# Optimization experiments

Hardware: AMD Instinct MI355X
Metric: run time of the kernel (lower is better)

The kernel has to match this reference:

```python
import jax, jax.numpy as jnp
import numpy as np

N = 2_000_000   # total flattened logits (anchors x classes scale)
FG = 256        # number of foreground (targets==1) entries
DELTA = 1.0


def setup_inputs() -> dict:
    key = jax.random.key(0)
    k1, k2 = jax.random.split(key)
    logits = jax.random.normal(k1, (N,), dtype=jnp.float32)
    fg_idx = jax.random.choice(k2, N, shape=(FG,), replace=False)
    targets = jnp.zeros((N,), dtype=jnp.int32).at[fg_idx].set(1)
    return {"logits": logits, "targets": targets, "fg_num": FG}


def _ap_loss(logits, targets, fg_num):
    """Faithful port of AP_loss: returns (loss [1], grad [N]).

    The torch validity filter (targets==0 & logits >= min(fg)-delta) is
    redundant: for invalid bg, (l - fg_i)/(2*delta)+0.5 < 0, so clamp gives 0.
    We therefore mask with (targets==0) over the full array (static shapes).
    """
    bg_mask = (targets == 0).astype(logits.dtype)
    fg_idx = jnp.nonzero(targets == 1, size=fg_num)[0]
    fg_logits = logits[fg_idx]            # [fg]
    order = jnp.argsort(fg_logits)
    sorted_fg = fg_logits[order]          # ascending, matches torch loop order

    inv2d = 1.0 / (2.0 * DELTA)

    def step(carry, f_i):
        max_prec, bg_grad = carry
        tmp1 = jnp.clip((fg_logits - f_i) * inv2d + 0.5, 0.0, 1.0)   # [fg]
        tmp2 = jnp.clip((logits - f_i) * inv2d + 0.5, 0.0, 1.0) * bg_mask  # [N]
        a = jnp.sum(tmp1) + 0.5
        b = jnp.sum(tmp2)
        cur = a / (a + b)
        new_max = jnp.maximum(max_prec, cur)
        scale = jnp.where(max_prec <= cur, 1.0, (1.0 - max_prec) / (1.0 - cur))
        bg_grad = bg_grad + tmp2 * (scale / (a + b))
        return (new_max, bg_grad), new_max

    init = (jnp.zeros((), logits.dtype), jnp.zeros_like(logits))
    (_, bg_grad), prec_sorted = jax.lax.scan(step, init, sorted_fg)

    prec = jnp.zeros((fg_num,), logits.dtype).at[order].set(prec_sorted)
    grad = bg_grad.at[fg_idx].set(-(1.0 - prec))
    denom = max(fg_num, 1)
    grad = grad / denom
    metric = jnp.sum(prec, keepdims=True) / denom   # [1]
    return 1.0 - metric, grad


def reference(logits, targets, fg_num):
    loss, _ = _ap_loss(logits, targets, fg_num)
    return loss
```

## Files before the change

### kernel.cpp

```cpp
#include <hip/hip_runtime.h>

#define FG    256
#define NBIN  1024
#define BINV  32.0f
#define BOFF  512.0f
#define NBLK  256

typedef unsigned long long u64;
typedef unsigned int u32;


__global__ void __launch_bounds__(1024) hist_kernel(
        const float* __restrict__ logits,
        const int* __restrict__ targets,
        float* __restrict__ fgslots,
        int* __restrict__ fgcnt,
        u32* __restrict__ partials, int n) {
    __shared__ u32 h[NBIN];
    __shared__ float lfg[FG];
    __shared__ int lcnt;
    const int tid = threadIdx.x;
    h[tid] = 0u;
    if (tid == 0) lcnt = 0;
    __syncthreads();

    const int n4 = n >> 2;
    const float4* l4 = (const float4*)logits;
    const int4*   t4 = (const int4*)targets;
    const int stride = gridDim.x * blockDim.x;
    for (int i = blockIdx.x * blockDim.x + tid; i < n4; i += stride) {
        float4 x = l4[i];
        int4   t = t4[i];
        #pragma unroll
        for (int e = 0; e < 4; ++e) {
            float l  = (e == 0) ? x.x : (e == 1) ? x.y : (e == 2) ? x.z : x.w;
            int   tg = (e == 0) ? t.x : (e == 1) ? t.y : (e == 2) ? t.z : t.w;
            float u = fmaf(l, BINV, BOFF);
            u = fminf(fmaxf(u, 0.f), 1023.99f);
            int b = (int)u;
            u32 qoff = (u32)((u - (float)b) * 32.0f);
            atomicAdd(&h[b], (1u << 18) | qoff);
            if (tg == 1) {
                int p = atomicAdd(&lcnt, 1);
                if (p < FG) lfg[p] = l;
            }
        }
    }
    if (blockIdx.x == 0 && tid == 0) {
        for (int i = n4 << 2; i < n; ++i) {
            float l = logits[i];
            float u = fmaf(l, BINV, BOFF);
            u = fminf(fmaxf(u, 0.f), 1023.99f);
            int b = (int)u;
            u32 qoff = (u32)((u - (float)b) * 32.0f);
            atomicAdd(&h[b], (1u << 18) | qoff);
            if (targets[i] == 1) {
                int p = atomicAdd(&lcnt, 1);
                if (p < FG) lfg[p] = l;
            }
        }
    }
    __syncthreads();
    partials[blockIdx.x * NBIN + tid] = h[tid];
    const int c = (lcnt < FG) ? lcnt : FG;
    if (tid == 0) fgcnt[blockIdx.x] = c;
    if (tid < c) fgslots[blockIdx.x * FG + tid] = lfg[tid];
}

__global__ void __launch_bounds__(1024) final_kernel(
        const int* __restrict__ fgcnt,
        const float* __restrict__ fgslots,
        const u32* __restrict__ partials,
        float* __restrict__ out, int n) {
    __shared__ float rc[NBIN], rs[NBIN];
    __shared__ float pc[NBIN], ps[NBIN];
    __shared__ float sfv[FG], sf[FG];
    __shared__ int   pr[1024];
    __shared__ float pa[1024];
    __shared__ float wc[16], ws[16];
    __shared__ float wm[4], wsum[4];
    __shared__ u32   ucnt[NBIN], uqs[NBIN];
    __shared__ int   fwp[4];
    const int tid  = threadIdx.x;
    const int lane = tid & 63;
    const int wv   = tid >> 6;

    ucnt[tid] = 0u; uqs[tid] = 0u;
    int fv = (tid < FG) ? fgcnt[tid] : 0;
    __syncthreads();

    {
        const uint4* p4 = (const uint4*)partials;
        u32 c0=0,c1=0,c2=0,c3=0,q0=0,q1=0,q2=0,q3=0;
        #pragma unroll 8
        for (int k = 0; k < 64; ++k) {
            uint4 v = p4[tid + (k << 10)];
            c0 += v.x >> 18; q0 += v.x & 0x3FFFFu;
            c1 += v.y >> 18; q1 += v.y & 0x3FFFFu;
            c2 += v.z >> 18; q2 += v.z & 0x3FFFFu;
            c3 += v.w >> 18; q3 += v.w & 0x3FFFFu;
        }
        const int bb = (tid & 255) << 2;
        atomicAdd(&ucnt[bb + 0], c0); atomicAdd(&uqs[bb + 0], q0);
        atomicAdd(&ucnt[bb + 1], c1); atomicAdd(&uqs[bb + 1], q1);
        atomicAdd(&ucnt[bb + 2], c2); atomicAdd(&uqs[bb + 2], q2);
        atomicAdd(&ucnt[bb + 3], c3); atomicAdd(&uqs[bb + 3], q3);
    }
    int fs = fv;
    if (tid < FG) {
        #pragma unroll
        for (int off = 1; off < 64; off <<= 1) {
            int t = __shfl_up(fs, off, 64);
            if (lane >= off) fs += t;
        }
        if (lane == 63) fwp[wv] = fs;
    }
    __syncthreads();

    {
        float cnt = (float)ucnt[tid];
        float qs  = (float)uqs[tid];
        float binlo = ((float)tid - BOFF) * (1.0f / BINV);
        rc[tid] = cnt;
        rs[tid] = fmaf(qs + 0.5f * cnt, 1.0f / 1024.0f, binlo * cnt);
    }
    if (tid < FG) {
        int excl = fs - fv;
        for (int w = 0; w < wv; ++w) excl += fwp[w];
        for (int j = 0; j < fv; ++j) sfv[excl + j] = fgslots[tid * FG + j];
    }
    __syncthreads();

    float c = rc[tid], s = rs[tid];
    #pragma unroll
    for (int off = 1; off < 64; off <<= 1) {
        float tc = __shfl_up(c, off, 64), ts = __shfl_up(s, off, 64);
        if (lane >= off) { c += tc; s += ts; }
    }
    if (lane == 63) { wc[wv] = c; ws[wv] = s; }

    {
        int i = tid & 255, ch = tid >> 8;
        float v = sfv[i];
        int r = 0;
        #pragma unroll 8
        for (int j = ch * 64; j < ch * 64 + 64; ++j) {
            float o = sfv[j];
            r += (o < v || (o == v && j < i)) ? 1 : 0;
        }
        pr[tid] = r;
    }
    __syncthreads();

    if (wv == 0 && lane < 16) {
        float cc = wc[lane], ss = ws[lane];
        #pragma unroll
        for (int off = 1; off < 16; off <<= 1) {
            float tc = __shfl_up(cc, off, 64), ts = __shfl_up(ss, off, 64);
            if (lane >= off) { cc += tc; ss += ts; }
        }
        wc[lane] = cc; ws[lane] = ss;
    }
    if (tid < FG) {
        int r = pr[tid] + pr[tid + 256] + pr[tid + 512] + pr[tid + 768];
        sf[r] = sfv[tid];
    }
    __syncthreads();
    if (wv > 0) { c += wc[wv - 1]; s += ws[wv - 1]; }
    pc[tid] = c; ps[tid] = s;

    {
        int i = tid & 255, ch = tid >> 8;
        float fi = sf[i];
        float sum = 0.f;
        #pragma unroll 8
        for (int j = ch * 64; j < ch * 64 + 64; ++j) {
            float v = (sf[j] - fi) * 0.5f + 0.5f;
            sum += fminf(fmaxf(v, 0.f), 1.f);
        }
        pa[tid] = sum;
    }
    __syncthreads();

    float cur = 0.f;
    if (tid < FG) {
        const float fi = sf[tid];
        const float a = 0.5f + pa[tid] + pa[tid + 256] + pa[tid + 512] + pa[tid + 768];
        float C[2], S[2];
        #pragma unroll
        for (int q = 0; q < 2; ++q) {
            float t = (q == 0) ? (fi - 1.0f) : (fi + 1.0f);
            float u = fmaf(t, BINV, BOFF);
            u = fminf(fmaxf(u, 0.f), 1023.99f);
            float kf = floorf(u);
            int   k  = (int)kf;
            float frac = u - kf;
            C[q] = pc[k] + rc[k] * (frac - 1.0f);
            S[q] = ps[k] + rs[k] * (frac - 1.0f);
        }
        const float Cab   = (float)n - C[1];
        const float Cw    = C[1] - C[0];
        const float Sw    = S[1] - S[0];
        const float b_all = Cab + 0.5f * Sw + (0.5f - 0.5f * fi) * Cw;
        const float b_bg  = b_all - (a - 0.5f);
        cur = a / (a + b_bg);
        float m = cur;
        #pragma unroll
        for (int off = 1; off < 64; off <<= 1) {
            float t = __shfl_up(m, off, 64);
            if (lane >= off) m = fmaxf(m, t);
        }
        if (lane == 63) wm[wv] = m;
        pr[tid] = __float_as_int(m);
    }
    __syncthreads();
    if (tid < FG) {
        float m = __int_as_float(pr[tid]);
        float pmax = -1.f;
        for (int w = 0; w < 4; ++w) if (w < wv) pmax = fmaxf(pmax, wm[w]);
        m = fmaxf(m, pmax);
        float v = m;
        #pragma unroll
        for (int off = 32; off; off >>= 1) v += __shfl_down(v, off, 64);
        if (lane == 0) wsum[wv] = v;
    }
    __syncthreads();
    if (tid == 0) {
        float t = (wsum[0] + wsum[1]) + (wsum[2] + wsum[3]);
        out[0] = 1.f - t / (float)FG;
    }
}

extern "C" void kernel_launch(void* const* d_in, const int* in_sizes, int n_in,
                              void* d_out, int out_size, void* d_ws, size_t ws_size,
                              hipStream_t stream) {
    const float* logits  = (const float*)d_in[0];
    const int*   targets = (const int*)d_in[1];
    const int n = in_sizes[0];

    char*  wb       = (char*)d_ws;
    int*   fgcnt    = (int*)wb;
    float* fgslots  = (float*)(wb + 4096);
    u32*   partials = (u32*)(wb + (1 << 20));
    float* out      = (float*)d_out;

    hist_kernel<<<NBLK, 1024, 0, stream>>>(logits, targets, fgslots, fgcnt, partials, n);
    final_kernel<<<1, 1024, 0, stream>>>(fgcnt, fgslots, partials, out, n);
}
```

Baseline: 85.91 us.

## Fuse histogram and final reduction into one cooperative kernel with grid syncs

```diff
diff --git a/kernel.cpp b/kernel.cpp
--- a/kernel.cpp
+++ b/kernel.cpp
@@ -1,4 +1,7 @@
 #include <hip/hip_runtime.h>
+#include <hip/hip_cooperative_groups.h>
+
+namespace cg = cooperative_groups;
 
 #define FG    256
 #define NBIN  1024
@@ -10,16 +13,32 @@
 typedef unsigned int u32;
 
 
-__global__ void __launch_bounds__(1024) hist_kernel(
+__global__ void __launch_bounds__(1024) ap_fused(
         const float* __restrict__ logits,
         const int* __restrict__ targets,
         float* __restrict__ fgslots,
         int* __restrict__ fgcnt,
-        u32* __restrict__ partials, int n) {
+        u32* __restrict__ partials,
+        u64* __restrict__ gacc,
+        float* __restrict__ out, int n) {
     __shared__ u32 h[NBIN];
     __shared__ float lfg[FG];
     __shared__ int lcnt;
-    const int tid = threadIdx.x;
+    __shared__ u32 redc[4][4], redq[4][4];
+    __shared__ float rc[NBIN], rs[NBIN];
+    __shared__ float pc[NBIN], ps[NBIN];
+    __shared__ float sfv[FG], sf[FG];
+    __shared__ int   pr[1024];
+    __shared__ float pa[1024];
+    __shared__ float wcs[16], wss[16];
+    __shared__ float wm[4], wsum[4];
+    __shared__ int   fwp[4];
+
+    const int tid  = threadIdx.x;
+    const int lane = tid & 63;
+    const int wv   = tid >> 6;
+    const int g    = blockIdx.x;
+
     h[tid] = 0u;
     if (tid == 0) lcnt = 0;
     __syncthreads();
@@ -28,7 +47,7 @@
     const float4* l4 = (const float4*)logits;
     const int4*   t4 = (const int4*)targets;
     const int stride = gridDim.x * blockDim.x;
-    for (int i = blockIdx.x * blockDim.x + tid; i < n4; i += stride) {
+    for (int i = g * blockDim.x + tid; i < n4; i += stride) {
         float4 x = l4[i];
         int4   t = t4[i];
         #pragma unroll
@@ -46,7 +65,7 @@
             }
         }
     }
-    if (blockIdx.x == 0 && tid == 0) {
+    if (g == 0 && tid == 0) {
         for (int i = n4 << 2; i < n; ++i) {
             float l = logits[i];
             float u = fmaf(l, BINV, BOFF);
@@ -61,51 +80,54 @@
         }
     }
     __syncthreads();
-    partials[blockIdx.x * NBIN + tid] = h[tid];
-    const int c = (lcnt < FG) ? lcnt : FG;
-    if (tid == 0) fgcnt[blockIdx.x] = c;
-    if (tid < c) fgslots[blockIdx.x * FG + tid] = lfg[tid];
-}
-
-__global__ void __launch_bounds__(1024) final_kernel(
-        const int* __restrict__ fgcnt,
-        const float* __restrict__ fgslots,
-        const u32* __restrict__ partials,
-        float* __restrict__ out, int n) {
-    __shared__ float rc[NBIN], rs[NBIN];
-    __shared__ float pc[NBIN], ps[NBIN];
-    __shared__ float sfv[FG], sf[FG];
-    __shared__ int   pr[1024];
-    __shared__ float pa[1024];
-    __shared__ float wc[16], ws[16];
-    __shared__ float wm[4], wsum[4];
-    __shared__ u32   ucnt[NBIN], uqs[NBIN];
-    __shared__ int   fwp[4];
-    const int tid  = threadIdx.x;
-    const int lane = tid & 63;
-    const int wv   = tid >> 6;
-
-    ucnt[tid] = 0u; uqs[tid] = 0u;
+    partials[g * NBIN + tid] = h[tid];
+    const int c_ = (lcnt < FG) ? lcnt : FG;
+    if (tid == 0) fgcnt[g] = c_;
+    if (tid < c_) fgslots[g * FG + tid] = lfg[tid];
+
+    cg::this_grid().sync();
+
+    if (tid < 256) {
+        const uint4* p4 = (const uint4*)partials;
+        uint4 v = p4[tid * (NBIN / 4) + g];
+        u32 c0 = v.x >> 18, q0 = v.x & 0x3FFFFu;
+        u32 c1 = v.y >> 18, q1 = v.y & 0x3FFFFu;
+        u32 c2 = v.z >> 18, q2 = v.z & 0x3FFFFu;
+        u32 c3 = v.w >> 18, q3 = v.w & 0x3FFFFu;
+        #pragma unroll
+        for (int off = 32; off; off >>= 1) {
+            c0 += __shfl_down(c0, off, 64); q0 += __shfl_down(q0, off, 64);
+            c1 += __shfl_down(c1, off, 64); q1 += __shfl_down(q1, off, 64);
+            c2 += __shfl_down(c2, off, 64); q2 += __shfl_down(q2, off, 64);
+            c3 += __shfl_down(c3, off, 64); q3 += __shfl_down(q3, off, 64);
+        }
+        if (lane == 0) {
+            redc[wv][0] = c0; redq[wv][0] = q0;
+            redc[wv][1] = c1; redq[wv][1] = q1;
+            redc[wv][2] = c2; redq[wv][2] = q2;
+            redc[wv][3] = c3; redq[wv][3] = q3;
+        }
+    }
+    __syncthreads();
+    if (tid < 4) {
+        u32 cnt = redc[0][tid] + redc[1][tid] + redc[2][tid] + redc[3][tid];
+        u32 qs  = redq[0][tid] + redq[1][tid] + redq[2][tid] + redq[3][tid];
+        gacc[4 * g + tid] = ((u64)cnt << 32) | (u64)qs;
+    }
+
+    cg::this_grid().sync();
+
+    if (g != 0) return;
+
+    {
+        u64 v = gacc[tid];
+        float cnt = (float)(u32)(v >> 32);
+        float qs  = (float)(u32)(v & 0xFFFFFFFFull);
+        float binlo = ((float)tid - BOFF) * (1.0f / BINV);
+        rc[tid] = cnt;
+        rs[tid] = fmaf(qs + 0.5f * cnt, 1.0f / 1024.0f, binlo * cnt);
+    }
     int fv = (tid < FG) ? fgcnt[tid] : 0;
-    __syncthreads();
-
-    {
-        const uint4* p4 = (const uint4*)partials;
-        u32 c0=0,c1=0,c2=0,c3=0,q0=0,q1=0,q2=0,q3=0;
-        #pragma unroll 8
-        for (int k = 0; k < 64; ++k) {
-            uint4 v = p4[tid + (k << 10)];
-            c0 += v.x >> 18; q0 += v.x & 0x3FFFFu;
-            c1 += v.y >> 18; q1 += v.y & 0x3FFFFu;
-            c2 += v.z >> 18; q2 += v.z & 0x3FFFFu;
-            c3 += v.w >> 18; q3 += v.w & 0x3FFFFu;
-        }
-        const int bb = (tid & 255) << 2;
-        atomicAdd(&ucnt[bb + 0], c0); atomicAdd(&uqs[bb + 0], q0);
-        atomicAdd(&ucnt[bb + 1], c1); atomicAdd(&uqs[bb + 1], q1);
-        atomicAdd(&ucnt[bb + 2], c2); atomicAdd(&uqs[bb + 2], q2);
-        atomicAdd(&ucnt[bb + 3], c3); atomicAdd(&uqs[bb + 3], q3);
-    }
     int fs = fv;
     if (tid < FG) {
         #pragma unroll
@@ -116,14 +138,6 @@
         if (lane == 63) fwp[wv] = fs;
     }
     __syncthreads();
-
-    {
-        float cnt = (float)ucnt[tid];
-        float qs  = (float)uqs[tid];
-        float binlo = ((float)tid - BOFF) * (1.0f / BINV);
-        rc[tid] = cnt;
-        rs[tid] = fmaf(qs + 0.5f * cnt, 1.0f / 1024.0f, binlo * cnt);
-    }
     if (tid < FG) {
         int excl = fs - fv;
         for (int w = 0; w < wv; ++w) excl += fwp[w];
@@ -137,7 +151,7 @@
         float tc = __shfl_up(c, off, 64), ts = __shfl_up(s, off, 64);
         if (lane >= off) { c += tc; s += ts; }
     }
-    if (lane == 63) { wc[wv] = c; ws[wv] = s; }
+    if (lane == 63) { wcs[wv] = c; wss[wv] = s; }
 
     {
         int i = tid & 255, ch = tid >> 8;
@@ -153,20 +167,20 @@
     __syncthreads();
 
     if (wv == 0 && lane < 16) {
-        float cc = wc[lane], ss = ws[lane];
+        float cc = wcs[lane], ss = wss[lane];
         #pragma unroll
         for (int off = 1; off < 16; off <<= 1) {
             float tc = __shfl_up(cc, off, 64), ts = __shfl_up(ss, off, 64);
             if (lane >= off) { cc += tc; ss += ts; }
         }
-        wc[lane] = cc; ws[lane] = ss;
+        wcs[lane] = cc; wss[lane] = ss;
     }
     if (tid < FG) {
         int r = pr[tid] + pr[tid + 256] + pr[tid + 512] + pr[tid + 768];
         sf[r] = sfv[tid];
     }
     __syncthreads();
-    if (wv > 0) { c += wc[wv - 1]; s += ws[wv - 1]; }
+    if (wv > 0) { c += wcs[wv - 1]; s += wss[wv - 1]; }
     pc[tid] = c; ps[tid] = s;
 
     {
@@ -236,14 +250,17 @@
                               hipStream_t stream) {
     const float* logits  = (const float*)d_in[0];
     const int*   targets = (const int*)d_in[1];
-    const int n = in_sizes[0];
+    int n = in_sizes[0];
 
     char*  wb       = (char*)d_ws;
     int*   fgcnt    = (int*)wb;
     float* fgslots  = (float*)(wb + 4096);
     u32*   partials = (u32*)(wb + (1 << 20));
+    u64*   gacc     = (u64*)(wb + (1 << 21));
     float* out      = (float*)d_out;
 
-    hist_kernel<<<NBLK, 1024, 0, stream>>>(logits, targets, fgslots, fgcnt, partials, n);
-    final_kernel<<<1, 1024, 0, stream>>>(fgcnt, fgslots, partials, out, n);
+    void* args[] = { &logits, &targets, &fgslots, &fgcnt,
+                     &partials, &gacc, &out, &n };
+    hipLaunchCooperativeKernel((void*)ap_fused, dim3(NBLK), dim3(1024),
+                               args, 0, stream);
 }
```

Result: slower. 140.2 us (+63.2%).

## Split histogram partial reduction into a separate 16-block kernel

Applied to the files above, without the earlier changes.

```diff
diff --git a/kernel.cpp b/kernel.cpp
--- a/kernel.cpp
+++ b/kernel.cpp
@@ -67,45 +67,62 @@
     if (tid < c) fgslots[blockIdx.x * FG + tid] = lfg[tid];
 }
 
+__global__ void __launch_bounds__(1024) reduce_kernel(
+        const u32* __restrict__ partials,
+        u64* __restrict__ gacc) {
+    __shared__ u32 sc[16 * 64], sq[16 * 64];
+    const int tid = threadIdx.x;
+    const int b  = tid & 63;
+    const int r0 = tid >> 6;
+    const int g  = blockIdx.x;
+
+    u32 cs = 0, qs = 0;
+    #pragma unroll
+    for (int k = 0; k < 16; ++k) {
+        u32 v = partials[(r0 + (k << 4)) * NBIN + (g << 6) + b];
+        cs += v >> 18;
+        qs += v & 0x3FFFFu;
+    }
+    sc[r0 * 64 + b] = cs;
+    sq[r0 * 64 + b] = qs;
+    __syncthreads();
+    if (tid < 64) {
+        u32 c = 0, q = 0;
+        #pragma unroll
+        for (int r = 0; r < 16; ++r) {
+            c += sc[r * 64 + tid];
+            q += sq[r * 64 + tid];
+        }
+        gacc[(g << 6) + tid] = ((u64)c << 32) | (u64)q;
+    }
+}
+
 __global__ void __launch_bounds__(1024) final_kernel(
         const int* __restrict__ fgcnt,
         const float* __restrict__ fgslots,
-        const u32* __restrict__ partials,
+        const u64* __restrict__ gacc,
         float* __restrict__ out, int n) {
     __shared__ float rc[NBIN], rs[NBIN];
     __shared__ float pc[NBIN], ps[NBIN];
     __shared__ float sfv[FG], sf[FG];
     __shared__ int   pr[1024];
     __shared__ float pa[1024];
-    __shared__ float wc[16], ws[16];
+    __shared__ float wcs[16], wss[16];
     __shared__ float wm[4], wsum[4];
-    __shared__ u32   ucnt[NBIN], uqs[NBIN];
     __shared__ int   fwp[4];
     const int tid  = threadIdx.x;
     const int lane = tid & 63;
     const int wv   = tid >> 6;
 
-    ucnt[tid] = 0u; uqs[tid] = 0u;
+    {
+        u64 v = gacc[tid];
+        float cnt = (float)(u32)(v >> 32);
+        float qs  = (float)(u32)(v & 0xFFFFFFFFull);
+        float binlo = ((float)tid - BOFF) * (1.0f / BINV);
+        rc[tid] = cnt;
+        rs[tid] = fmaf(qs + 0.5f * cnt, 1.0f / 1024.0f, binlo * cnt);
+    }
     int fv = (tid < FG) ? fgcnt[tid] : 0;
-    __syncthreads();
-
-    {
-        const uint4* p4 = (const uint4*)partials;
-        u32 c0=0,c1=0,c2=0,c3=0,q0=0,q1=0,q2=0,q3=0;
-        #pragma unroll 8
-        for (int k = 0; k < 64; ++k) {
-            uint4 v = p4[tid + (k << 10)];
-            c0 += v.x >> 18; q0 += v.x & 0x3FFFFu;
-            c1 += v.y >> 18; q1 += v.y & 0x3FFFFu;
-            c2 += v.z >> 18; q2 += v.z & 0x3FFFFu;
-            c3 += v.w >> 18; q3 += v.w & 0x3FFFFu;
-        }
-        const int bb = (tid & 255) << 2;
-        atomicAdd(&ucnt[bb + 0], c0); atomicAdd(&uqs[bb + 0], q0);
-        atomicAdd(&ucnt[bb + 1], c1); atomicAdd(&uqs[bb + 1], q1);
-        atomicAdd(&ucnt[bb + 2], c2); atomicAdd(&uqs[bb + 2], q2);
-        atomicAdd(&ucnt[bb + 3], c3); atomicAdd(&uqs[bb + 3], q3);
-    }
     int fs = fv;
     if (tid < FG) {
         #pragma unroll
@@ -116,14 +133,6 @@
         if (lane == 63) fwp[wv] = fs;
     }
     __syncthreads();
-
-    {
-        float cnt = (float)ucnt[tid];
-        float qs  = (float)uqs[tid];
-        float binlo = ((float)tid - BOFF) * (1.0f / BINV);
-        rc[tid] = cnt;
-        rs[tid] = fmaf(qs + 0.5f * cnt, 1.0f / 1024.0f, binlo * cnt);
-    }
     if (tid < FG) {
         int excl = fs - fv;
         for (int w = 0; w < wv; ++w) excl += fwp[w];
@@ -137,7 +146,7 @@
         float tc = __shfl_up(c, off, 64), ts = __shfl_up(s, off, 64);
         if (lane >= off) { c += tc; s += ts; }
     }
-    if (lane == 63) { wc[wv] = c; ws[wv] = s; }
+    if (lane == 63) { wcs[wv] = c; wss[wv] = s; }
 
     {
         int i = tid & 255, ch = tid >> 8;
@@ -153,20 +162,20 @@
     __syncthreads();
 
     if (wv == 0 && lane < 16) {
-        float cc = wc[lane], ss = ws[lane];
+        float cc = wcs[lane], ss = wss[lane];
         #pragma unroll
         for (int off = 1; off < 16; off <<= 1) {
             float tc = __shfl_up(cc, off, 64), ts = __shfl_up(ss, off, 64);
             if (lane >= off) { cc += tc; ss += ts; }
         }
-        wc[lane] = cc; ws[lane] = ss;
+        wcs[lane] = cc; wss[lane] = ss;
     }
     if (tid < FG) {
         int r = pr[tid] + pr[tid + 256] + pr[tid + 512] + pr[tid + 768];
         sf[r] = sfv[tid];
     }
     __syncthreads();
-    if (wv > 0) { c += wc[wv - 1]; s += ws[wv - 1]; }
+    if (wv > 0) { c += wcs[wv - 1]; s += wss[wv - 1]; }
     pc[tid] = c; ps[tid] = s;
 
     {
@@ -242,8 +251,10 @@
     int*   fgcnt    = (int*)wb;
     float* fgslots  = (float*)(wb + 4096);
     u32*   partials = (u32*)(wb + (1 << 20));
+    u64*   gacc     = (u64*)(wb + (1 << 21));
     float* out      = (float*)d_out;
 
     hist_kernel<<<NBLK, 1024, 0, stream>>>(logits, targets, fgslots, fgcnt, partials, n);
-    final_kernel<<<1, 1024, 0, stream>>>(fgcnt, fgslots, partials, out, n);
-}
+    reduce_kernel<<<16, 1024, 0, stream>>>(partials, gacc);
+    final_kernel<<<1, 1024, 0, stream>>>(fgcnt, fgslots, gacc, out, n);
+}
```

Result: faster. 77.97 us (-9.2%).
